# Kernel optimization log

Hardware: AMD Instinct MI355X
Metric: run time of the kernel (lower is better)

## Reference

```python
import jax, jax.numpy as jnp
import numpy as np

B, T, C, H, W = 2, 4, 3, 96, 96
HF, L = 128, 6
TC = T * C
EPS = 1e-5


def swish(x):
    return x * jax.nn.sigmoid(x)


def _build_edges(h, w):
    # self-loops + 8-neighbor grid edges, exactly as image_to_graph
    edges = [np.stack([np.arange(h * w)] * 2)]
    nx0, ny0 = np.meshgrid(np.arange(w), np.arange(h), indexing='ij')
    for dx, dy in [(-1, -1), (0, -1), (1, -1), (-1, 0), (1, 0), (-1, 1), (0, 1), (1, 1)]:
        nx, ny = nx0 + dx, ny0 + dy
        src = ny * w + nx
        dst = (ny - dy) * w + (nx - dx)
        ok = (nx >= 0) & (nx < w) & (0 <= ny) & (ny < h)
        edges.append(np.stack([src[ok], dst[ok]]))
    return np.concatenate(edges, axis=1)


def setup_inputs() -> dict:
    key = jax.random.key(0)
    ks = iter(jax.random.split(key, 40))

    def lin(fi, fo):
        return jax.random.normal(next(ks), (fi, fo), jnp.float32) / np.sqrt(fi).astype(np.float32)

    x = jax.random.normal(next(ks), (B, T, C, H, W), jnp.float32)
    ei = _build_edges(H, W)
    px, py = np.meshgrid(np.arange(W), np.arange(H), indexing='ij')
    pos = np.stack([px.flatten(), py.flatten()], 1).astype(np.float32) / (H - 1)
    return dict(
        x=x,
        edge_src=jnp.asarray(ei[0], jnp.int32),
        edge_dst=jnp.asarray(ei[1], jnp.int32),
        pos=jnp.asarray(pos),
        emb_w1=lin(TC + 2, HF), emb_b1=jnp.zeros((HF,), jnp.float32),
        emb_w2=lin(HF, HF), emb_b2=jnp.zeros((HF,), jnp.float32),
        msg_w1=jnp.stack([lin(2 * HF + TC + 1, HF) for _ in range(L)]),
        msg_b1=jnp.zeros((L, HF), jnp.float32),
        msg_w2=jnp.stack([lin(HF, HF) for _ in range(L)]),
        msg_b2=jnp.zeros((L, HF), jnp.float32),
        upd_w1=jnp.stack([lin(2 * HF, HF) for _ in range(L)]),
        upd_b1=jnp.zeros((L, HF), jnp.float32),
        upd_w2=jnp.stack([lin(HF, HF) for _ in range(L)]),
        upd_b2=jnp.zeros((L, HF), jnp.float32),
        out_w1=lin(HF, HF), out_b1=jnp.zeros((HF,), jnp.float32),
        out_w2=lin(HF, C), out_b2=jnp.zeros((C,), jnp.float32),
    )


def _forward(x, emb_w1, emb_b1, emb_w2, emb_b2, msg_w1, msg_b1, msg_w2, msg_b2,
             upd_w1, upd_b1, upd_w2, upd_b2, out_w1, out_b1, out_w2, out_b2,
             edge_src, edge_dst, pos):
    b, t, c, h, w = x.shape
    n = h * w
    u = x.reshape(b, t * c, n).transpose(0, 2, 1)                       # [B,N,TC]
    node_in = jnp.concatenate([u, jnp.broadcast_to(pos, (b, n, 2))], -1)
    hf = swish(swish(node_in @ emb_w1 + emb_b1) @ emb_w2 + emb_b2)      # [B,N,HF]
    dist = jnp.linalg.norm(pos[edge_dst] - pos[edge_src], axis=1, keepdims=True)  # [E,1]
    dist_b = jnp.broadcast_to(dist, (b,) + dist.shape)
    deg = jnp.zeros((n,), x.dtype).at[edge_dst].add(1.0)                # >=1 (self loops)
    for l in range(msg_w1.shape[0]):
        m_in = jnp.concatenate([hf[:, edge_dst], hf[:, edge_src],
                                u[:, edge_dst] - u[:, edge_src], dist_b], -1)
        m = swish(swish(m_in @ msg_w1[l] + msg_b1[l]) @ msg_w2[l] + msg_b2[l])
        agg = jnp.zeros(hf.shape, hf.dtype).at[:, edge_dst].add(m) / deg[None, :, None]
        upd = swish(swish(jnp.concatenate([hf, agg], -1) @ upd_w1[l] + upd_b1[l])
                    @ upd_w2[l] + upd_b2[l])
        hf = hf + upd                                                    # residual (in==out)
        mu = hf.mean(axis=1, keepdims=True)                              # InstanceNorm per graph
        var = hf.var(axis=1, keepdims=True)
        hf = (hf - mu) * jax.lax.rsqrt(var + EPS)
    hg = hf.reshape(b, h, w, -1)
    diff = (swish(hg @ out_w1 + out_b1) @ out_w2 + out_b2).transpose(0, 3, 1, 2)
    return (x[:, -1] + diff)[:, None]                                    # [B,1,C,H,W]


def reference(x, edge_src, edge_dst, pos, emb_w1, emb_b1, emb_w2, emb_b2,
              msg_w1, msg_b1, msg_w2, msg_b2, upd_w1, upd_b1, upd_w2, upd_b2,
              out_w1, out_b1, out_w2, out_b2):
    return _forward(x, emb_w1, emb_b1, emb_w2, emb_b2, msg_w1, msg_b1, msg_w2, msg_b2,
                    upd_w1, upd_b1, upd_w2, upd_b2, out_w1, out_b1, out_w2, out_b2,
                    edge_src, edge_dst, pos)
```

## Files before the change

kernel.cpp:

```cpp
#include <hip/hip_runtime.h>
#include <hip/hip_bf16.h>
#include <math.h>

#define HF 128
#define NB 9216
#define BB 2
#define MROWS (BB*NB)
#define GH 96
#define GW 96
#define LAYERS 6

typedef __attribute__((ext_vector_type(8))) short bf16x8;
typedef __attribute__((ext_vector_type(4))) float f32x4;

#define MFMA16(a, b, c) __builtin_amdgcn_mfma_f32_16x16x32_bf16(a, b, c, 0, 0, 0)

__device__ __forceinline__ float swishf(float x) {
    return __fdividef(x, 1.0f + __expf(-x));
}

__device__ __forceinline__ unsigned short f2b(float f) {
    __hip_bfloat16 h = __float2bfloat16(f);
    return *reinterpret_cast<unsigned short*>(&h);
}
__device__ __forceinline__ unsigned pk2(float lo, float hi) {
    return (unsigned)f2b(lo) | ((unsigned)f2b(hi) << 16);
}
__device__ __forceinline__ float b2f(unsigned short u) {
    return __uint_as_float((unsigned)u << 16);
}

__device__ __forceinline__ bf16x8 norm_frag(const float* __restrict__ hp,
                                            const float* __restrict__ mus,
                                            const float* __restrict__ rss, int k0) {
    float4 h0 = *(const float4*)hp;
    float4 h1 = *(const float4*)(hp + 4);
    float4 m0 = *(const float4*)&mus[k0];
    float4 m1 = *(const float4*)&mus[k0 + 4];
    float4 r0 = *(const float4*)&rss[k0];
    float4 r1 = *(const float4*)&rss[k0 + 4];
    union { bf16x8 v; unsigned u[4]; } az;
    az.u[0] = pk2((h0.x - m0.x) * r0.x, (h0.y - m0.y) * r0.y);
    az.u[1] = pk2((h0.z - m0.z) * r0.z, (h0.w - m0.w) * r0.w);
    az.u[2] = pk2((h1.x - m1.x) * r1.x, (h1.y - m1.y) * r1.y);
    az.u[3] = pk2((h1.z - m1.z) * r1.z, (h1.w - m1.w) * r1.w);
    return az.v;
}

__device__ __forceinline__ void load_musig(const float* __restrict__ mraw, int b, int t,
                                           float* __restrict__ mus, float* __restrict__ rss) {
    if (t < 128) {
        float mu = 0.f, rs = 1.f;
        if (mraw) {
            float s = mraw[b * 128 + t], q = mraw[256 + b * 128 + t];
            mu = s * (1.0f / NB);
            float var = q * (1.0f / NB) - mu * mu;
            rs = rsqrtf(var + 1e-5f);
        }
        mus[t] = mu; rss[t] = rs;
    }
}

__global__ void k_prep(const float* __restrict__ embw2, const float* __restrict__ outw1,
                       const float* __restrict__ msgw1, const float* __restrict__ msgw2,
                       const float* __restrict__ updw1, const float* __restrict__ updw2,
                       unsigned short* __restrict__ wT) {
    int s = blockIdx.x;
    const float* src;
    if (s == 0) src = embw2;
    else if (s == 1) src = outw1;
    else {
        int l = (s - 2) / 6, r = (s - 2) % 6;
        if (r == 0)      src = msgw1 + (size_t)l * 269 * HF;
        else if (r == 1) src = msgw1 + (size_t)l * 269 * HF + HF * HF;
        else if (r == 2) src = msgw2 + (size_t)l * HF * HF;
        else if (r == 3) src = updw1 + (size_t)l * 256 * HF;
        else if (r == 4) src = updw1 + (size_t)l * 256 * HF + HF * HF;
        else             src = updw2 + (size_t)l * HF * HF;
    }
    __shared__ float tile[128][133];
    int t = threadIdx.x;
#pragma unroll
    for (int i = 0; i < 64; ++i) {
        int id = i * 256 + t;
        tile[id >> 7][id & 127] = src[id];
    }
    __syncthreads();
    unsigned short* o = wT + (size_t)s * 16384;
#pragma unroll
    for (int i = 0; i < 64; ++i) {
        int id = i * 256 + t;
        int col = id >> 7, k = id & 127;
        o[id] = f2b(tile[k][col]);
    }
}

__global__ void k_build(const float* __restrict__ x, const float* __restrict__ pos,
                        float* __restrict__ nodein, float* __restrict__ msr) {
    int idx = blockIdx.x * 256 + threadIdx.x;
    if (idx < LAYERS * 512) msr[idx] = 0.0f;
    if (idx >= MROWS) return;
    int b = idx / NB, n = idx - b * NB;
    float* o = nodein + (size_t)idx * 16;
    const float* xb = x + (size_t)b * 12 * NB + n;
#pragma unroll
    for (int k = 0; k < 12; ++k) o[k] = xb[(size_t)k * NB];
    o[12] = pos[2 * n];
    o[13] = pos[2 * n + 1];
    o[14] = 0.0f; o[15] = 0.0f;
}

__global__ __launch_bounds__(256, 4)
void k_emb(const float* __restrict__ nodein, const float* __restrict__ w1,
           const float* __restrict__ b1, const unsigned short* __restrict__ wT2,
           const float* __restrict__ b2, float* __restrict__ hf) {
    __shared__ float xs[16][14];
    __shared__ char t1s[4096];
    int t = threadIdx.x;
    int rt = blockIdx.x * 16;
    if (t < 224) {
        int r = t / 14, k = t - r * 14;
        xs[r][k] = nodein[(size_t)(rt + r) * 16 + k];
    }
    __syncthreads();
    {
        int f = t & 127, rblk = t >> 7;
        float wreg[14];
#pragma unroll
        for (int k = 0; k < 14; ++k) wreg[k] = w1[k * HF + f];
        float bv = b1[f];
#pragma unroll
        for (int i = 0; i < 8; ++i) {
            int row = rblk * 8 + i;
            float acc = bv;
#pragma unroll
            for (int k = 0; k < 14; ++k) acc = fmaf(xs[row][k], wreg[k], acc);
            int addr = (row * 256 + f * 2) ^ ((row & 7) << 4);
            *(unsigned short*)(t1s + addr) = f2b(swishf(acc));
        }
    }
    __syncthreads();
    int wave = t >> 6, lane = t & 63, lr = lane & 15, lg = lane >> 4;
    int fb = wave * 32;
    f32x4 acc[2];
    acc[0] = (f32x4)0.0f; acc[1] = (f32x4)0.0f;
#pragma unroll
    for (int kc = 0; kc < 4; ++kc) {
        int k0 = kc * 32 + lg * 8;
        bf16x8 a = *(const bf16x8*)(t1s + ((lr * 256 + k0 * 2) ^ ((lr & 7) << 4)));
#pragma unroll
        for (int j = 0; j < 2; ++j) {
            bf16x8 b = *(const bf16x8*)(wT2 + (size_t)(fb + j * 16 + lr) * HF + k0);
            acc[j] = MFMA16(a, b, acc[j]);
        }
    }
#pragma unroll
    for (int j = 0; j < 2; ++j) {
        int f = fb + j * 16 + lr;
        float bv = b2[f];
#pragma unroll
        for (int r = 0; r < 4; ++r) {
            size_t o = (size_t)(rt + lg * 4 + r) * HF + f;
            hf[o] = swishf(acc[j][r] + bv);
        }
    }
}

__global__ __launch_bounds__(256, 4)
void k_as(const float* __restrict__ hf, const float* __restrict__ mraw,
          const unsigned short* __restrict__ wA, const unsigned short* __restrict__ wB,
          const float* __restrict__ nodein, const float* __restrict__ w1u,
          unsigned short* __restrict__ A, unsigned short* __restrict__ S) {
    __shared__ float w1s[12][128];
    __shared__ float nis[16][12];
    __shared__ float mus[128], rss[128];
    int t = threadIdx.x, wave = t >> 6, lane = t & 63, lr = lane & 15, lg = lane >> 4;
    int rt = blockIdx.x * 16;
    int b = blockIdx.x / (NB / 16);
    int fb = wave * 32;
    for (int i = t; i < 12 * 128; i += 256) w1s[i >> 7][i & 127] = w1u[i];
    if (t < 192) {
        int r = t / 12, k = t - (t / 12) * 12;
        nis[r][k] = nodein[(size_t)(rt + r) * 16 + k];
    }
    load_musig(mraw, b, t, mus, rss);
    __syncthreads();
    f32x4 accA[2], accS[2];
    accA[0] = (f32x4)0.0f; accA[1] = (f32x4)0.0f;
    accS[0] = (f32x4)0.0f; accS[1] = (f32x4)0.0f;
#pragma unroll
    for (int kc = 0; kc < 4; ++kc) {
        int k0 = kc * 32 + lg * 8;
        bf16x8 a = norm_frag(hf + (size_t)(rt + lr) * HF + k0, mus, rss, k0);
#pragma unroll
        for (int j = 0; j < 2; ++j) {
            bf16x8 bA = *(const bf16x8*)(wA + (size_t)(fb + j * 16 + lr) * HF + k0);
            accA[j] = MFMA16(a, bA, accA[j]);
            bf16x8 bS = *(const bf16x8*)(wB + (size_t)(fb + j * 16 + lr) * HF + k0);
            accS[j] = MFMA16(a, bS, accS[j]);
        }
    }
#pragma unroll
    for (int j = 0; j < 2; ++j) {
        int f = fb + j * 16 + lr;
        float au[4] = {0.f, 0.f, 0.f, 0.f};
#pragma unroll
        for (int k = 0; k < 12; ++k) {
            float wv = w1s[k][f];
#pragma unroll
            for (int r = 0; r < 4; ++r) au[r] = fmaf(nis[lg * 4 + r][k], wv, au[r]);
        }
#pragma unroll
        for (int r = 0; r < 4; ++r) {
            size_t o = (size_t)(rt + lg * 4 + r) * HF + f;
            A[o] = f2b(accA[j][r] + au[r]);
            S[o] = f2b(accS[j][r] - au[r]);
        }
    }
}

__global__ __launch_bounds__(256, 4)
void k_aggupd(const unsigned short* __restrict__ Ab, const unsigned short* __restrict__ Sb,
              const unsigned short* __restrict__ wT2, const float* __restrict__ b2m,
              const float* __restrict__ b1m, const float* __restrict__ w1d,
              float* __restrict__ hf, const float* __restrict__ mraw,
              const unsigned short* __restrict__ w1a, const unsigned short* __restrict__ w1b,
              const unsigned short* __restrict__ w2u, const float* __restrict__ b1u,
              const float* __restrict__ b2u, float* __restrict__ msr) {
    __shared__ float dsb[3][128];
    __shared__ float mus[128], rss[128];
    __shared__ char exb[3 * 4096];
    int t = threadIdx.x, kq = t >> 6, lane = t & 63, lr = lane & 15, lg = lane >> 4;
    int bx = blockIdx.x;
    int b = bx / (NB / 16), tile = bx % (NB / 16);
    int rt = tile * 16;
    int fb = kq * 32;
    size_t bN = (size_t)b * NB;
    int R = rt / GW, C0 = rt % GW;

    if (t < 128) {
        float bb = b1m[t], wd = w1d[t];
        dsb[0][t] = bb;
        dsb[1][t] = fmaf(1.0f / 95.0f, wd, bb);
        dsb[2][t] = fmaf(1.4142135623730951f / 95.0f, wd, bb);
    }
    load_musig(mraw, b, t, mus, rss);
    bf16x8 w2f[2][4];
#pragma unroll
    for (int j = 0; j < 2; ++j)
#pragma unroll
        for (int kc = 0; kc < 4; ++kc)
            w2f[j][kc] = *(const bf16x8*)(wT2 + (size_t)(fb + j * 16 + lr) * HF
                                          + kc * 32 + lg * 8);
    int rowA = rt + lr;
    float Af[8];
    {
        bf16x8 av = *(const bf16x8*)(Ab + (bN + rowA) * HF + kq * 32 + lg * 8);
#pragma unroll
        for (int e = 0; e < 8; ++e) Af[e] = b2f((unsigned short)av[e]);
    }
    float b2r[2] = { b2m[fb + lr], b2m[fb + 16 + lr] };
    int lofs = lane * 16;
    bool mC[3][4];
#pragma unroll
    for (int dcI = 0; dcI < 3; ++dcI)
#pragma unroll
        for (int r = 0; r < 4; ++r)
            mC[dcI][r] = (unsigned)(C0 + lg * 4 + r + dcI - 1) < (unsigned)GW;
    __syncthreads();

    f32x4 agg2[2];
    agg2[0] = (f32x4)0.0f; agg2[1] = (f32x4)0.0f;
    bf16x8 sv;
    {
        int src = min(max(rowA - 97, 0), NB - 1);
        sv = *(const bf16x8*)(Sb + (bN + src) * HF + kq * 32 + lg * 8);
    }
#pragma unroll 1
    for (int g = 0; g < 3; ++g) {
        int dr = g - 1;
        bool rOK = (unsigned)(R + dr) < (unsigned)GH;
#pragma unroll
        for (int oi = 0; oi < 3; ++oi) {
            int off = g * 3 + oi;
            int dc = oi - 1;
            int dd = dr * dr + dc * dc;
            bf16x8 cur = sv;
            if (off < 8) {
                int no = off + 1;
                int dnn = (no / 3 - 1) * GW + (no % 3 - 1);
                int src = min(max(rowA + dnn, 0), NB - 1);
                sv = *(const bf16x8*)(Sb + (bN + src) * HF + kq * 32 + lg * 8);
            }
            const float* dp = &dsb[dd][kq * 32 + lg * 8];
            union { bf16x8 v; unsigned u[4]; } cu; cu.v = cur;
            union { bf16x8 v; unsigned u[4]; } az;
#pragma unroll
            for (int q = 0; q < 4; ++q) {
                float sl = __uint_as_float(cu.u[q] << 16);
                float sh = __uint_as_float(cu.u[q] & 0xffff0000u);
                float zl = swishf(Af[2 * q]     + sl + dp[2 * q]);
                float zh = swishf(Af[2 * q + 1] + sh + dp[2 * q + 1]);
                az.u[q] = pk2(zl, zh);
            }
            *(bf16x8*)(exb + oi * 4096 + kq * 1024 + lofs) = az.v;
        }
        __syncthreads();
#pragma unroll
        for (int oi = 0; oi < 3; ++oi) {
            f32x4 acc[2];
            acc[0] = (f32x4)0.0f; acc[1] = (f32x4)0.0f;
#pragma unroll
            for (int kc = 0; kc < 4; ++kc) {
                bf16x8 a = *(const bf16x8*)(exb + oi * 4096 + kc * 1024 + lofs);
                acc[0] = MFMA16(a, w2f[0][kc], acc[0]);
                acc[1] = MFMA16(a, w2f[1][kc], acc[1]);
            }
#pragma unroll
            for (int j = 0; j < 2; ++j)
#pragma unroll
                for (int r = 0; r < 4; ++r) {
                    if (rOK && mC[oi][r])
                        agg2[j][r] += swishf(acc[j][r] + b2r[j]);
                }
        }
        __syncthreads();
    }

    float nr = 1.0f + (R > 0) + (R < GH - 1);
#pragma unroll
    for (int j = 0; j < 2; ++j)
#pragma unroll
        for (int r = 0; r < 4; ++r) {
            int row = lg * 4 + r;
            int C = C0 + row;
            float nc = 1.0f + (C > 0) + (C < GW - 1);
            float v = __fdividef(agg2[j][r], nr * nc);
            int f = fb + j * 16 + lr;
            int addr = (row * 256 + f * 2) ^ ((row & 7) << 4);
            *(unsigned short*)(exb + addr) = f2b(v);
        }
    __syncthreads();

    f32x4 acc[2];
    acc[0] = (f32x4)0.0f; acc[1] = (f32x4)0.0f;
#pragma unroll
    for (int kc = 0; kc < 4; ++kc) {
        int k0 = kc * 32 + lg * 8;
        bf16x8 a1 = norm_frag(hf + (bN + rt + lr) * HF + k0, mus, rss, k0);
        bf16x8 a2 = *(const bf16x8*)(exb + ((lr * 256 + k0 * 2) ^ ((lr & 7) << 4)));
#pragma unroll
        for (int j = 0; j < 2; ++j) {
            bf16x8 bA = *(const bf16x8*)(w1a + (size_t)(fb + j * 16 + lr) * HF + k0);
            acc[j] = MFMA16(a1, bA, acc[j]);
            bf16x8 bB = *(const bf16x8*)(w1b + (size_t)(fb + j * 16 + lr) * HF + k0);
            acc[j] = MFMA16(a2, bB, acc[j]);
        }
    }
#pragma unroll
    for (int j = 0; j < 2; ++j) {
        int col = fb + j * 16 + lr;
        float bv = b1u[col];
#pragma unroll
        for (int r = 0; r < 4; ++r) {
            int row = lg * 4 + r;
            int addr = (row * 256 + col * 2) ^ ((row & 7) << 4);
            *(unsigned short*)(exb + 4096 + addr) = f2b(swishf(acc[j][r] + bv));
        }
    }
    __syncthreads();
    f32x4 acc2[2];
    acc2[0] = (f32x4)0.0f; acc2[1] = (f32x4)0.0f;
#pragma unroll
    for (int kc = 0; kc < 4; ++kc) {
        int k0 = kc * 32 + lg * 8;
        bf16x8 a = *(const bf16x8*)(exb + 4096 + ((lr * 256 + k0 * 2) ^ ((lr & 7) << 4)));
#pragma unroll
        for (int j = 0; j < 2; ++j) {
            bf16x8 bfr = *(const bf16x8*)(w2u + (size_t)(fb + j * 16 + lr) * HF + k0);
            acc2[j] = MFMA16(a, bfr, acc2[j]);
        }
    }
#pragma unroll
    for (int j = 0; j < 2; ++j) {
        int f = fb + j * 16 + lr;
        float bv = b2u[f];
        float mu = mus[f], rs = rss[f];
        float s1 = 0.f, s2 = 0.f;
#pragma unroll
        for (int r = 0; r < 4; ++r) {
            size_t o = (bN + rt + lg * 4 + r) * HF + f;
            float v = swishf(acc2[j][r] + bv) + (hf[o] - mu) * rs;
            hf[o] = v;
            s1 += v; s2 += v * v;
        }
        s1 += __shfl_xor(s1, 16); s1 += __shfl_xor(s1, 32);
        s2 += __shfl_xor(s2, 16); s2 += __shfl_xor(s2, 32);
        if (lg == 0) {
            atomicAdd(&msr[b * 128 + f], s1);
            atomicAdd(&msr[256 + b * 128 + f], s2);
        }
    }
}

__global__ __launch_bounds__(256, 4)
void k_out(const float* __restrict__ hf, const float* __restrict__ mraw,
           const unsigned short* __restrict__ wT1, const float* __restrict__ b1,
           const float* __restrict__ w2, const float* __restrict__ b2,
           const float* __restrict__ x, float* __restrict__ out) {
    __shared__ float g1s[16][132];
    __shared__ float w2s[384];
    __shared__ float mus[128], rss[128];
    int t = threadIdx.x, wave = t >> 6, lane = t & 63, lr = lane & 15, lg = lane >> 4;
    int rt = blockIdx.x * 16;
    int b = blockIdx.x / (NB / 16);
    int fb = wave * 32;
    for (int i = t; i < 384; i += 256) w2s[i] = w2[i];
    load_musig(mraw, b, t, mus, rss);
    __syncthreads();
    f32x4 acc[2];
    acc[0] = (f32x4)0.0f; acc[1] = (f32x4)0.0f;
#pragma unroll
    for (int kc = 0; kc < 4; ++kc) {
        int k0 = kc * 32 + lg * 8;
        bf16x8 a = norm_frag(hf + (size_t)(rt + lr) * HF + k0, mus, rss, k0);
#pragma unroll
        for (int j = 0; j < 2; ++j) {
            bf16x8 bfr = *(const bf16x8*)(wT1 + (size_t)(fb + j * 16 + lr) * HF + k0);
            acc[j] = MFMA16(a, bfr, acc[j]);
        }
    }
#pragma unroll
    for (int j = 0; j < 2; ++j) {
        int f = fb + j * 16 + lr;
        float bv = b1[f];
#pragma unroll
        for (int r = 0; r < 4; ++r)
            g1s[lg * 4 + r][f] = swishf(acc[j][r] + bv);
    }
    __syncthreads();
    if (t < 48) {
        int r = t / 3, c = t - (t / 3) * 3;
        int row = rt + r;
        int bb = row / NB, n = row - bb * NB;
        float a = b2[c];
#pragma unroll 8
        for (int k = 0; k < HF; ++k) a = fmaf(g1s[r][k], w2s[k * 3 + c], a);
        float xv = x[(((size_t)bb * 4 + 3) * 3 + c) * NB + n];
        out[((size_t)bb * 3 + c) * NB + n] = a + xv;
    }
}

extern "C" void kernel_launch(void* const* d_in, const int* in_sizes, int n_in,
                              void* d_out, int out_size, void* d_ws, size_t ws_size,
                              hipStream_t stream) {
    const float* x      = (const float*)d_in[0];
    const float* pos    = (const float*)d_in[3];
    const float* emb_w1 = (const float*)d_in[4];
    const float* emb_b1 = (const float*)d_in[5];
    const float* emb_b2 = (const float*)d_in[7];
    const float* msg_w1 = (const float*)d_in[8];
    const float* msg_b1 = (const float*)d_in[9];
    const float* msg_b2 = (const float*)d_in[11];
    const float* upd_b1 = (const float*)d_in[13];
    const float* upd_b2 = (const float*)d_in[15];
    const float* out_b1 = (const float*)d_in[17];
    const float* out_w2 = (const float*)d_in[18];
    const float* out_b2 = (const float*)d_in[19];

    float* w = (float*)d_ws;
    size_t off = 0;
    auto alloc = [&](size_t n) { float* p = w + off; off += n; return p; };
    float* nodein  = alloc((size_t)MROWS * 16);
    float* hf      = alloc((size_t)MROWS * HF);
    float* msr     = alloc((size_t)LAYERS * 512);
    unsigned short* Abf  = (unsigned short*)alloc((size_t)MROWS * 64);
    unsigned short* Sbf  = (unsigned short*)alloc((size_t)MROWS * 64);
    unsigned short* wT   = (unsigned short*)alloc((size_t)38 * 16384 / 2);
    (void)ws_size; (void)in_sizes; (void)n_in; (void)out_size;

    k_prep<<<38, 256, 0, stream>>>((const float*)d_in[6], (const float*)d_in[16],
                                   msg_w1, (const float*)d_in[10],
                                   (const float*)d_in[12], (const float*)d_in[14], wT);
    k_build<<<(MROWS + 255) / 256, 256, 0, stream>>>(x, pos, nodein, msr);
    k_emb<<<1152, 256, 0, stream>>>(nodein, emb_w1, emb_b1, wT + 0 * 16384, emb_b2, hf);
    for (int l = 0; l < LAYERS; ++l) {
        const unsigned short* wL = wT + (size_t)(2 + 6 * l) * 16384;
        const float* W1 = msg_w1 + (size_t)l * 269 * HF;
        const float* mprev = (l == 0) ? nullptr : msr + (size_t)(l - 1) * 512;
        k_as<<<1152, 256, 0, stream>>>(hf, mprev, wL + 0 * 16384, wL + 1 * 16384,
                                       nodein, W1 + 256 * HF, Abf, Sbf);
        k_aggupd<<<1152, 256, 0, stream>>>(Abf, Sbf, wL + 2 * 16384, msg_b2 + l * HF,
                                           msg_b1 + l * HF, W1 + 268 * HF,
                                           hf, mprev,
                                           wL + 3 * 16384, wL + 4 * 16384,
                                           wL + 5 * 16384, upd_b1 + l * HF,
                                           upd_b2 + l * HF, msr + (size_t)l * 512);
    }
    k_out<<<1152, 256, 0, stream>>>(hf, msr + (size_t)(LAYERS - 1) * 512,
                                    wT + 1 * 16384, out_b1, out_w2, out_b2,
                                    x, (float*)d_out);
}
```

Measured before the change: 456.9 us.

## Double-buffer edge activation tiles and fold bias/distance terms into registers

The aggregation-update kernel now double-buffers its shared-memory tile of per-edge activations, so the swish activations for the next neighbour row group are computed while MFMAs run on the current one. This removes one barrier per group. The per-distance bias terms are precomputed into registers together with the node's A row, which drops the shared dsb table and its loads. Neighbour source indices are hoisted up front. In exchange the kernel uses about twice the LDS for the tile and keeps 24 extra float registers, which may reduce occupancy under launch_bounds(256,4).

```diff
diff --git a/kernel.cpp b/kernel.cpp
--- a/kernel.cpp
+++ b/kernel.cpp
@@ -227,9 +227,8 @@
               const unsigned short* __restrict__ w1a, const unsigned short* __restrict__ w1b,
               const unsigned short* __restrict__ w2u, const float* __restrict__ b1u,
               const float* __restrict__ b2u, float* __restrict__ msr) {
-    __shared__ float dsb[3][128];
     __shared__ float mus[128], rss[128];
-    __shared__ char exb[3 * 4096];
+    __shared__ char exb[2 * 12288];
     int t = threadIdx.x, kq = t >> 6, lane = t & 63, lr = lane & 15, lg = lane >> 4;
     int bx = blockIdx.x;
     int b = bx / (NB / 16), tile = bx % (NB / 16);
@@ -238,12 +237,6 @@
     size_t bN = (size_t)b * NB;
     int R = rt / GW, C0 = rt % GW;
 
-    if (t < 128) {
-        float bb = b1m[t], wd = w1d[t];
-        dsb[0][t] = bb;
-        dsb[1][t] = fmaf(1.0f / 95.0f, wd, bb);
-        dsb[2][t] = fmaf(1.4142135623730951f / 95.0f, wd, bb);
-    }
     load_musig(mraw, b, t, mus, rss);
     bf16x8 w2f[2][4];
 #pragma unroll
@@ -253,12 +246,30 @@
             w2f[j][kc] = *(const bf16x8*)(wT2 + (size_t)(fb + j * 16 + lr) * HF
                                           + kc * 32 + lg * 8);
     int rowA = rt + lr;
-    float Af[8];
+    int kbase = kq * 32 + lg * 8;
+    float AfD[3][8];
     {
-        bf16x8 av = *(const bf16x8*)(Ab + (bN + rowA) * HF + kq * 32 + lg * 8);
-#pragma unroll
-        for (int e = 0; e < 8; ++e) Af[e] = b2f((unsigned short)av[e]);
-    }
+        bf16x8 av = *(const bf16x8*)(Ab + (bN + rowA) * HF + kbase);
+        float4 b1lo = *(const float4*)&b1m[kbase], b1hi = *(const float4*)&b1m[kbase + 4];
+        float4 wdlo = *(const float4*)&w1d[kbase], wdhi = *(const float4*)&w1d[kbase + 4];
+        const float c1 = 1.0f / 95.0f, c2 = 1.4142135623730951f / 95.0f;
+        float bb[8] = {b1lo.x, b1lo.y, b1lo.z, b1lo.w, b1hi.x, b1hi.y, b1hi.z, b1hi.w};
+        float wd[8] = {wdlo.x, wdlo.y, wdlo.z, wdlo.w, wdhi.x, wdhi.y, wdhi.z, wdhi.w};
+#pragma unroll
+        for (int e = 0; e < 8; ++e) {
+            float a = b2f((unsigned short)av[e]);
+            AfD[0][e] = a + bb[e];
+            AfD[1][e] = a + fmaf(c1, wd[e], bb[e]);
+            AfD[2][e] = a + fmaf(c2, wd[e], bb[e]);
+        }
+    }
+    int srcr[9];
+#pragma unroll
+    for (int off = 0; off < 9; ++off) {
+        int dn = (off / 3 - 1) * GW + (off % 3 - 1);
+        srcr[off] = min(max(rowA + dn, 0), NB - 1);
+    }
+    const unsigned short* Sbase = Sb + bN * HF + kbase;
     float b2r[2] = { b2m[fb + lr], b2m[fb + 16 + lr] };
     int lofs = lane * 16;
     bool mC[3][4];
@@ -267,52 +278,42 @@
 #pragma unroll
         for (int r = 0; r < 4; ++r)
             mC[dcI][r] = (unsigned)(C0 + lg * 4 + r + dcI - 1) < (unsigned)GW;
-    __syncthreads();
-
-    f32x4 agg2[2];
-    agg2[0] = (f32x4)0.0f; agg2[1] = (f32x4)0.0f;
-    bf16x8 sv;
-    {
-        int src = min(max(rowA - 97, 0), NB - 1);
-        sv = *(const bf16x8*)(Sb + (bN + src) * HF + kq * 32 + lg * 8);
-    }
-#pragma unroll 1
-    for (int g = 0; g < 3; ++g) {
-        int dr = g - 1;
-        bool rOK = (unsigned)(R + dr) < (unsigned)GH;
+
+    auto zgroup = [&](int g, char* buf) {
 #pragma unroll
         for (int oi = 0; oi < 3; ++oi) {
             int off = g * 3 + oi;
-            int dc = oi - 1;
-            int dd = dr * dr + dc * dc;
-            bf16x8 cur = sv;
-            if (off < 8) {
-                int no = off + 1;
-                int dnn = (no / 3 - 1) * GW + (no % 3 - 1);
-                int src = min(max(rowA + dnn, 0), NB - 1);
-                sv = *(const bf16x8*)(Sb + (bN + src) * HF + kq * 32 + lg * 8);
-            }
-            const float* dp = &dsb[dd][kq * 32 + lg * 8];
+            int dd = (g - 1) * (g - 1) + (oi - 1) * (oi - 1);
+            bf16x8 cur = *(const bf16x8*)(Sbase + (size_t)srcr[off] * HF);
             union { bf16x8 v; unsigned u[4]; } cu; cu.v = cur;
             union { bf16x8 v; unsigned u[4]; } az;
 #pragma unroll
             for (int q = 0; q < 4; ++q) {
                 float sl = __uint_as_float(cu.u[q] << 16);
                 float sh = __uint_as_float(cu.u[q] & 0xffff0000u);
-                float zl = swishf(Af[2 * q]     + sl + dp[2 * q]);
-                float zh = swishf(Af[2 * q + 1] + sh + dp[2 * q + 1]);
-                az.u[q] = pk2(zl, zh);
+                az.u[q] = pk2(swishf(AfD[dd][2 * q] + sl),
+                              swishf(AfD[dd][2 * q + 1] + sh));
             }
-            *(bf16x8*)(exb + oi * 4096 + kq * 1024 + lofs) = az.v;
-        }
-        __syncthreads();
+            *(bf16x8*)(buf + oi * 4096 + kq * 1024 + lofs) = az.v;
+        }
+    };
+
+    f32x4 agg2[2];
+    agg2[0] = (f32x4)0.0f; agg2[1] = (f32x4)0.0f;
+    zgroup(0, exb);
+    __syncthreads();
+#pragma unroll 1
+    for (int g = 0; g < 3; ++g) {
+        char* curb = exb + (size_t)(g & 1) * 12288;
+        if (g < 2) zgroup(g + 1, exb + (size_t)((g + 1) & 1) * 12288);
+        bool rOK = (unsigned)(R + g - 1) < (unsigned)GH;
 #pragma unroll
         for (int oi = 0; oi < 3; ++oi) {
             f32x4 acc[2];
             acc[0] = (f32x4)0.0f; acc[1] = (f32x4)0.0f;
 #pragma unroll
             for (int kc = 0; kc < 4; ++kc) {
-                bf16x8 a = *(const bf16x8*)(exb + oi * 4096 + kc * 1024 + lofs);
+                bf16x8 a = *(const bf16x8*)(curb + oi * 4096 + kc * 1024 + lofs);
                 acc[0] = MFMA16(a, w2f[0][kc], acc[0]);
                 acc[1] = MFMA16(a, w2f[1][kc], acc[1]);
             }
```

New measurement: 504.9 us. 10.5% more time.

## Split k_aggupd across 8 waves with 16 output features each

Applied to the files above, without the earlier changes.

Doubles k_aggupd's block to 512 threads so each of 8 waves owns 16 output columns instead of 32, halving per-thread MFMA accumulators and weight fragments. The edge-message pre-activation stage is remapped so each thread handles 4 features of one row, stored to a swizzled LDS layout shared with the MFMA A-fragment reads. The aim is more waves per tile, lower register pressure and better latency hiding. The cost is more threads per block and more synchronisation, and each wave now reloads the A fragments from LDS for fewer MFMAs.

```diff
diff --git a/kernel.cpp b/kernel.cpp
--- a/kernel.cpp
+++ b/kernel.cpp
@@ -219,7 +219,7 @@
     }
 }
 
-__global__ __launch_bounds__(256, 4)
+__global__ __launch_bounds__(512)
 void k_aggupd(const unsigned short* __restrict__ Ab, const unsigned short* __restrict__ Sb,
               const unsigned short* __restrict__ wT2, const float* __restrict__ b2m,
               const float* __restrict__ b1m, const float* __restrict__ w1d,
@@ -230,11 +230,11 @@
     __shared__ float dsb[3][128];
     __shared__ float mus[128], rss[128];
     __shared__ char exb[3 * 4096];
-    int t = threadIdx.x, kq = t >> 6, lane = t & 63, lr = lane & 15, lg = lane >> 4;
+    int t = threadIdx.x, wave = t >> 6, lane = t & 63, lr = lane & 15, lg = lane >> 4;
     int bx = blockIdx.x;
     int b = bx / (NB / 16), tile = bx % (NB / 16);
     int rt = tile * 16;
-    int fb = kq * 32;
+    int fb = wave * 16;
     size_t bN = (size_t)b * NB;
     int R = rt / GW, C0 = rt % GW;
 
@@ -245,22 +245,22 @@
         dsb[2][t] = fmaf(1.4142135623730951f / 95.0f, wd, bb);
     }
     load_musig(mraw, b, t, mus, rss);
-    bf16x8 w2f[2][4];
-#pragma unroll
-    for (int j = 0; j < 2; ++j)
-#pragma unroll
-        for (int kc = 0; kc < 4; ++kc)
-            w2f[j][kc] = *(const bf16x8*)(wT2 + (size_t)(fb + j * 16 + lr) * HF
-                                          + kc * 32 + lg * 8);
-    int rowA = rt + lr;
-    float Af[8];
+    bf16x8 w2f[4];
+#pragma unroll
+    for (int kc = 0; kc < 4; ++kc)
+        w2f[kc] = *(const bf16x8*)(wT2 + (size_t)(fb + lr) * HF + kc * 32 + lg * 8);
+    int zrow = t >> 5, zk = (t & 31) * 4;
+    int zrowA = rt + zrow;
+    float Afz[4];
     {
-        bf16x8 av = *(const bf16x8*)(Ab + (bN + rowA) * HF + kq * 32 + lg * 8);
-#pragma unroll
-        for (int e = 0; e < 8; ++e) Af[e] = b2f((unsigned short)av[e]);
-    }
-    float b2r[2] = { b2m[fb + lr], b2m[fb + 16 + lr] };
-    int lofs = lane * 16;
+        unsigned short const* ap = Ab + (bN + zrowA) * HF + zk;
+        uint2 av = *(const uint2*)ap;
+        Afz[0] = __uint_as_float(av.x << 16);
+        Afz[1] = __uint_as_float(av.x & 0xffff0000u);
+        Afz[2] = __uint_as_float(av.y << 16);
+        Afz[3] = __uint_as_float(av.y & 0xffff0000u);
+    }
+    float b2w = b2m[fb + lr];
     bool mC[3][4];
 #pragma unroll
     for (int dcI = 0; dcI < 3; ++dcI)
@@ -269,128 +269,97 @@
             mC[dcI][r] = (unsigned)(C0 + lg * 4 + r + dcI - 1) < (unsigned)GW;
     __syncthreads();
 
-    f32x4 agg2[2];
-    agg2[0] = (f32x4)0.0f; agg2[1] = (f32x4)0.0f;
-    bf16x8 sv;
-    {
-        int src = min(max(rowA - 97, 0), NB - 1);
-        sv = *(const bf16x8*)(Sb + (bN + src) * HF + kq * 32 + lg * 8);
-    }
+    f32x4 agg2 = (f32x4)0.0f;
 #pragma unroll 1
     for (int g = 0; g < 3; ++g) {
         int dr = g - 1;
         bool rOK = (unsigned)(R + dr) < (unsigned)GH;
 #pragma unroll
         for (int oi = 0; oi < 3; ++oi) {
-            int off = g * 3 + oi;
             int dc = oi - 1;
             int dd = dr * dr + dc * dc;
-            bf16x8 cur = sv;
-            if (off < 8) {
-                int no = off + 1;
-                int dnn = (no / 3 - 1) * GW + (no % 3 - 1);
-                int src = min(max(rowA + dnn, 0), NB - 1);
-                sv = *(const bf16x8*)(Sb + (bN + src) * HF + kq * 32 + lg * 8);
+            int src = min(max(zrowA + dr * GW + dc, 0), NB - 1);
+            uint2 sv = *(const uint2*)(Sb + (bN + src) * HF + zk);
+            float4 dp = *(const float4*)&dsb[dd][zk];
+            float s0 = __uint_as_float(sv.x << 16);
+            float s1 = __uint_as_float(sv.x & 0xffff0000u);
+            float s2 = __uint_as_float(sv.y << 16);
+            float s3 = __uint_as_float(sv.y & 0xffff0000u);
+            uint2 p;
+            p.x = pk2(swishf(Afz[0] + s0 + dp.x), swishf(Afz[1] + s1 + dp.y));
+            p.y = pk2(swishf(Afz[2] + s2 + dp.z), swishf(Afz[3] + s3 + dp.w));
+            int addr = (zrow * 256 + zk * 2) ^ ((zrow & 7) << 4);
+            *(uint2*)(exb + oi * 4096 + addr) = p;
+        }
+        __syncthreads();
+#pragma unroll
+        for (int oi = 0; oi < 3; ++oi) {
+            f32x4 acc = (f32x4)0.0f;
+#pragma unroll
+            for (int kc = 0; kc < 4; ++kc) {
+                int k0 = kc * 32 + lg * 8;
+                bf16x8 a = *(const bf16x8*)(exb + oi * 4096 +
+                                            ((lr * 256 + k0 * 2) ^ ((lr & 7) << 4)));
+                acc = MFMA16(a, w2f[kc], acc);
             }
-            const float* dp = &dsb[dd][kq * 32 + lg * 8];
-            union { bf16x8 v; unsigned u[4]; } cu; cu.v = cur;
-            union { bf16x8 v; unsigned u[4]; } az;
-#pragma unroll
-            for (int q = 0; q < 4; ++q) {
-                float sl = __uint_as_float(cu.u[q] << 16);
-                float sh = __uint_as_float(cu.u[q] & 0xffff0000u);
-                float zl = swishf(Af[2 * q]     + sl + dp[2 * q]);
-                float zh = swishf(Af[2 * q + 1] + sh + dp[2 * q + 1]);
-                az.u[q] = pk2(zl, zh);
-            }
-            *(bf16x8*)(exb + oi * 4096 + kq * 1024 + lofs) = az.v;
+#pragma unroll
+            for (int r = 0; r < 4; ++r)
+                if (rOK && mC[oi][r])
+                    agg2[r] += swishf(acc[r] + b2w);
         }
         __syncthreads();
-#pragma unroll
-        for (int oi = 0; oi < 3; ++oi) {
-            f32x4 acc[2];
-            acc[0] = (f32x4)0.0f; acc[1] = (f32x4)0.0f;
-#pragma unroll
-            for (int kc = 0; kc < 4; ++kc) {
-                bf16x8 a = *(const bf16x8*)(exb + oi * 4096 + kc * 1024 + lofs);
-                acc[0] = MFMA16(a, w2f[0][kc], acc[0]);
-                acc[1] = MFMA16(a, w2f[1][kc], acc[1]);
-            }
-#pragma unroll
-            for (int j = 0; j < 2; ++j)
-#pragma unroll
-                for (int r = 0; r < 4; ++r) {
-                    if (rOK && mC[oi][r])
-                        agg2[j][r] += swishf(acc[j][r] + b2r[j]);
-                }
-        }
-        __syncthreads();
     }
 
     float nr = 1.0f + (R > 0) + (R < GH - 1);
 #pragma unroll
-    for (int j = 0; j < 2; ++j)
-#pragma unroll
-        for (int r = 0; r < 4; ++r) {
-            int row = lg * 4 + r;
-            int C = C0 + row;
-            float nc = 1.0f + (C > 0) + (C < GW - 1);
-            float v = __fdividef(agg2[j][r], nr * nc);
-            int f = fb + j * 16 + lr;
-            int addr = (row * 256 + f * 2) ^ ((row & 7) << 4);
-            *(unsigned short*)(exb + addr) = f2b(v);
-        }
-    __syncthreads();
-
-    f32x4 acc[2];
-    acc[0] = (f32x4)0.0f; acc[1] = (f32x4)0.0f;
+    for (int r = 0; r < 4; ++r) {
+        int row = lg * 4 + r;
+        int C = C0 + row;
+        float nc = 1.0f + (C > 0) + (C < GW - 1);
+        float v = __fdividef(agg2[r], nr * nc);
+        int addr = (row * 256 + (fb + lr) * 2) ^ ((row & 7) << 4);
+        *(unsigned short*)(exb + addr) = f2b(v);
+    }
+    __syncthreads();
+
+    f32x4 acc1 = (f32x4)0.0f;
 #pragma unroll
     for (int kc = 0; kc < 4; ++kc) {
         int k0 = kc * 32 + lg * 8;
         bf16x8 a1 = norm_frag(hf + (bN + rt + lr) * HF + k0, mus, rss, k0);
         bf16x8 a2 = *(const bf16x8*)(exb + ((lr * 256 + k0 * 2) ^ ((lr & 7) << 4)));
-#pragma unroll
-        for (int j = 0; j < 2; ++j) {
-            bf16x8 bA = *(const bf16x8*)(w1a + (size_t)(fb + j * 16 + lr) * HF + k0);
-            acc[j] = MFMA16(a1, bA, acc[j]);
-            bf16x8 bB = *(const bf16x8*)(w1b + (size_t)(fb + j * 16 + lr) * HF + k0);
-            acc[j] = MFMA16(a2, bB, acc[j]);
-        }
-    }
-#pragma unroll
-    for (int j = 0; j < 2; ++j) {
-        int col = fb + j * 16 + lr;
-        float bv = b1u[col];
+        bf16x8 bA = *(const bf16x8*)(w1a + (size_t)(fb + lr) * HF + k0);
+        acc1 = MFMA16(a1, bA, acc1);
+        bf16x8 bB = *(const bf16x8*)(w1b + (size_t)(fb + lr) * HF + k0);
+        acc1 = MFMA16(a2, bB, acc1);
+    }
+    {
+        float bv = b1u[fb + lr];
 #pragma unroll
         for (int r = 0; r < 4; ++r) {
             int row = lg * 4 + r;
-            int addr = (row * 256 + col * 2) ^ ((row & 7) << 4);
-            *(unsigned short*)(exb + 4096 + addr) = f2b(swishf(acc[j][r] + bv));
-        }
-    }
-    __syncthreads();
-    f32x4 acc2[2];
-    acc2[0] = (f32x4)0.0f; acc2[1] = (f32x4)0.0f;
+            int addr = (row * 256 + (fb + lr) * 2) ^ ((row & 7) << 4);
+            *(unsigned short*)(exb + 4096 + addr) = f2b(swishf(acc1[r] + bv));
+        }
+    }
+    __syncthreads();
+    f32x4 acc2 = (f32x4)0.0f;
 #pragma unroll
     for (int kc = 0; kc < 4; ++kc) {
         int k0 = kc * 32 + lg * 8;
         bf16x8 a = *(const bf16x8*)(exb + 4096 + ((lr * 256 + k0 * 2) ^ ((lr & 7) << 4)));
-#pragma unroll
-        for (int j = 0; j < 2; ++j) {
-            bf16x8 bfr = *(const bf16x8*)(w2u + (size_t)(fb + j * 16 + lr) * HF + k0);
-            acc2[j] = MFMA16(a, bfr, acc2[j]);
-        }
-    }
-#pragma unroll
-    for (int j = 0; j < 2; ++j) {
-        int f = fb + j * 16 + lr;
+        bf16x8 bw = *(const bf16x8*)(w2u + (size_t)(fb + lr) * HF + k0);
+        acc2 = MFMA16(a, bw, acc2);
+    }
+    {
+        int f = fb + lr;
         float bv = b2u[f];
         float mu = mus[f], rs = rss[f];
         float s1 = 0.f, s2 = 0.f;
 #pragma unroll
         for (int r = 0; r < 4; ++r) {
             size_t o = (bN + rt + lg * 4 + r) * HF + f;
-            float v = swishf(acc2[j][r] + bv) + (hf[o] - mu) * rs;
+            float v = swishf(acc2[r] + bv) + (hf[o] - mu) * rs;
             hf[o] = v;
             s1 += v; s2 += v * v;
         }
@@ -490,7 +459,7 @@
         const float* mprev = (l == 0) ? nullptr : msr + (size_t)(l - 1) * 512;
         k_as<<<1152, 256, 0, stream>>>(hf, mprev, wL + 0 * 16384, wL + 1 * 16384,
                                        nodein, W1 + 256 * HF, Abf, Sbf);
-        k_aggupd<<<1152, 256, 0, stream>>>(Abf, Sbf, wL + 2 * 16384, msg_b2 + l * HF,
+        k_aggupd<<<1152, 512, 0, stream>>>(Abf, Sbf, wL + 2 * 16384, msg_b2 + l * HF,
                                            msg_b1 + l * HF, W1 + 268 * HF,
                                            hf, mprev,
                                            wL + 3 * 16384, wL + 4 * 16384,
```

Measured after the change: 474.0 us. 1.04x slower.
